# Optimization experiments

Hardware: AMD Instinct MI355X
Metric: run time of the kernel (lower is better)

## Reference

```python
import jax, jax.numpy as jnp
import numpy as np

N, Z_DIM = 131072, 64
K_CODES = 2048
QUANT_TEMP = 0.0  # default T when 'quant_temp' not passed


def setup_inputs() -> dict:
    key = jax.random.key(0)
    k1, k2 = jax.random.split(key)
    z = jax.random.normal(k1, (N, Z_DIM), dtype=jnp.float32)
    e = jax.random.normal(k2, (K_CODES, Z_DIM), dtype=jnp.float32)
    return {"z": z, "e": e}


def reference(z, e):
    # torch.cdist -> euclidean distance matrix [N, K]; argmin over squared
    # distance gives identical indices (sqrt is monotone), so skip the sqrt.
    # ||z - e||^2 = ||z||^2 - 2 z.e^T + ||e||^2
    z_sq = jnp.sum(z * z, axis=1, keepdims=True)          # [N, 1]
    e_sq = jnp.sum(e * e, axis=1)                          # [K]
    d2 = z_sq - 2.0 * (z @ e.T) + e_sq[None, :]            # [N, K]
    min_indices = jnp.argmin(d2, axis=1)                   # [N] int
    z_q = e[min_indices]                                   # gather [N, Z]
    commit_loss = jnp.mean((z - z_q) ** 2)                 # F.mse_loss
    # straight-through: z + (1 - T) * stop_grad(z_q - z), T = 0
    z_out = z + (1.0 - QUANT_TEMP) * jax.lax.stop_gradient(z_q - z)
    return z_out, min_indices, commit_loss
```

## Files before the change

kernel.cpp:

```cpp
#include <hip/hip_runtime.h>


#define N_ROWS 131072
#define ZD 64
#define KCODES 2048
#define RF 4
#define EPS_S 0.02f
#define FLAG_CAP 65536
#define RFIX 8

using f16x8   = __attribute__((ext_vector_type(8))) _Float16;
using floatx4 = __attribute__((ext_vector_type(4))) float;


__global__ void prep_kernel(const float* __restrict__ e, float* __restrict__ ws) {
    int t = threadIdx.x, lane = t & 63, w = t >> 6;
    if (blockIdx.x == 0 && t == 0) { ws[0] = 0.0f; ((unsigned int*)ws)[1] = 0u; }
    int c = blockIdx.x * 4 + w;
    float* esn = ws + 1024;
    double* esq64 = (double*)((char*)ws + 16384);
    unsigned short* et = (unsigned short*)((char*)ws + 32768);
    float* eT = (float*)((char*)ws + 557056);

    float x = e[(size_t)c * ZD + lane];
    union { _Float16 h; unsigned short u; } cv;
    cv.h = (_Float16)x;
    int base = ((c >> 4) << 10) + ((lane >> 3) << 7) + ((c & 15) << 3) + (lane & 7);
    et[base] = cv.u;
    eT[lane * KCODES + c] = x;
    double s = (double)x * (double)x;
    for (int off = 1; off < 64; off <<= 1) s += __shfl_xor(s, off, 64);
    if (lane == 0) { esq64[c] = s; esn[c] = (float)(-0.5 * s); }
}

#define COMPUTE(H0, H1, EN, FCOL) do {                                       \
    floatx4 _ai = {EN, EN, EN, EN};                                          \
    _Pragma("unroll")                                                        \
    for (int _rf = 0; _rf < RF; _rf++) {                                     \
        floatx4 acc;                                                         \
        acc = __builtin_amdgcn_mfma_f32_16x16x32_f16(Fh[_rf][0], H0, _ai, 0, 0, 0); \
        acc = __builtin_amdgcn_mfma_f32_16x16x32_f16(Fh[_rf][1], H1, acc, 0, 0, 0); \
        _Pragma("unroll")                                                    \
        for (int _r = 0; _r < 4; _r++) {                                     \
            float _s  = acc[_r];                                             \
            bool  _gt = _s > mval[_rf][_r];                                  \
            mv2[_rf][_r]  = __builtin_amdgcn_fmed3f(_s, mval[_rf][_r], mv2[_rf][_r]); \
            midx[_rf][_r] = _gt ? (FCOL) : midx[_rf][_r];                    \
            mval[_rf][_r] = fmaxf(_s, mval[_rf][_r]);                        \
        }                                                                    \
    }                                                                        \
} while (0)

#define STAGEP(BUF, P) do {                                                  \
    const char* _src = etiles + ((size_t)((P) & 63) << 12)                   \
                       + ((size_t)threadIdx.x << 4);                         \
    __builtin_amdgcn_global_load_lds(                                        \
        (const __attribute__((address_space(1))) unsigned int*)_src,         \
        (__attribute__((address_space(3))) unsigned int*)&tilebuf[BUF][w << 10], \
        16, 0, 0);                                                           \
} while (0)

#define ITER_R(CT) do {                                                      \
    STAGEP(((CT) + 2) & 3, (CT) + 2);                                        \
    asm volatile("s_waitcnt vmcnt(2)" ::: "memory");                         \
    __builtin_amdgcn_s_barrier();                                            \
    float _en0 = esn_sm[(CT) * 32 + lrow];                                   \
    float _en1 = esn_sm[(CT) * 32 + 16 + lrow];                              \
    const char* _tb = tilebuf[(CT) & 3];                                     \
    f16x8 h0, h1;                                                            \
    h0 = *(const f16x8*)(const void*)(_tb + (lane << 4));                    \
    h1 = *(const f16x8*)(const void*)(_tb + 1024 + (lane << 4));             \
    COMPUTE(h0, h1, _en0, fcol);                                             \
    fcol += 16.0f;                                                           \
    h0 = *(const f16x8*)(const void*)(_tb + 2048 + (lane << 4));             \
    h1 = *(const f16x8*)(const void*)(_tb + 3072 + (lane << 4));             \
    COMPUTE(h0, h1, _en1, fcol);                                             \
    fcol += 16.0f;                                                           \
} while (0)

__global__ __launch_bounds__(256, 2) void vq_mfma(
        const float* __restrict__ z, const float* __restrict__ e,
        float* __restrict__ ws, float* __restrict__ out) {
    const char* etiles = (const char*)ws + 32768;
    unsigned int* cntp  = (unsigned int*)ws + 1;
    unsigned int* flags = (unsigned int*)((char*)ws + 294912);

    __shared__ __attribute__((aligned(16))) char tilebuf[4][4096];
    __shared__ __attribute__((aligned(16))) float esn_sm[KCODES];

    int lane = threadIdx.x & 63;
    int w    = threadIdx.x >> 6;
    int wid  = blockIdx.x * 4 + w;
    int row0 = wid * (RF * 16);
    int lrow = lane & 15;
    int lq   = lane >> 4;

    f16x8 Fh[RF][2];
#pragma unroll
    for (int rf = 0; rf < RF; rf++)
#pragma unroll
        for (int kc = 0; kc < 2; kc++) {
            const float* zp = z + (size_t)(row0 + rf * 16 + lrow) * ZD + kc * 32 + lq * 8;
            float xv[8];
            *(float4*)(void*)&xv[0] = *(const float4*)(const void*)zp;
            *(float4*)(void*)&xv[4] = *(const float4*)(const void*)(zp + 4);
            f16x8 h;
#pragma unroll
            for (int j = 0; j < 8; j++) h[j] = (_Float16)xv[j];
            Fh[rf][kc] = h;
            asm volatile("" : "+v"(Fh[rf][kc]));
        }
    asm volatile("s_waitcnt vmcnt(0)" ::: "memory");

    {
        const char* esrc = (const char*)ws + 4096 + ((size_t)threadIdx.x << 4);
        __builtin_amdgcn_global_load_lds(
            (const __attribute__((address_space(1))) unsigned int*)esrc,
            (__attribute__((address_space(3))) unsigned int*)((char*)esn_sm + (w << 10)),
            16, 0, 0);
        __builtin_amdgcn_global_load_lds(
            (const __attribute__((address_space(1))) unsigned int*)(esrc + 4096),
            (__attribute__((address_space(3))) unsigned int*)((char*)esn_sm + 4096 + (w << 10)),
            16, 0, 0);
    }
    STAGEP(0, 0);
    STAGEP(1, 1);

    floatx4 mval[RF], mv2[RF], midx[RF];
#pragma unroll
    for (int rf = 0; rf < RF; rf++)
#pragma unroll
        for (int r = 0; r < 4; r++) {
            mval[rf][r] = -3.0e38f; mv2[rf][r] = -3.0e38f; midx[rf][r] = 0.0f;
        }

    float fcol = (float)lrow;

    for (int ct = 0; ct < 64; ct += 4) {
        ITER_R(ct);
        ITER_R(ct + 1);
        ITER_R(ct + 2);
        ITER_R(ct + 3);
    }

    float lacc = 0.0f;
#pragma unroll
    for (int rf = 0; rf < RF; rf++)
#pragma unroll
        for (int r = 0; r < 4; r++) {
            float v = mval[rf][r], v2 = mv2[rf][r], fi = midx[rf][r];
            for (int off = 1; off < 16; off <<= 1) {
                float ov  = __shfl_xor(v,  off, 64);
                float ofi = __shfl_xor(fi, off, 64);
                float ov2 = __shfl_xor(v2, off, 64);
                bool take = (ov > v) || ((ov == v) && (ofi < fi));
                float loser = take ? v : ov;
                v2 = fmaxf(fmaxf(v2, ov2), loser);
                v  = take ? ov  : v;
                fi = take ? ofi : fi;
            }
            int row = row0 + rf * 16 + lq * 4 + r;
            int idx = (int)fi;
            float4 ev = ((const float4*)(const void*)(e + (size_t)idx * ZD))[lrow];
            float4 zv = ((const float4*)(const void*)(z + (size_t)row * ZD))[lrow];
            ((float4*)(void*)(out + (size_t)row * ZD))[lrow] = ev;
            float dx = ev.x - zv.x, dy = ev.y - zv.y;
            float dz = ev.z - zv.z, dw = ev.w - zv.w;
            lacc = fmaf(dx, dx, lacc); lacc = fmaf(dy, dy, lacc);
            lacc = fmaf(dz, dz, lacc); lacc = fmaf(dw, dw, lacc);
            if (lrow == 0) {
                out[(size_t)N_ROWS * ZD + row] = fi;
                if (v - v2 < EPS_S) {
                    unsigned int i = atomicAdd(cntp, 1u);
                    if (i < FLAG_CAP) flags[i] = (unsigned int)row;
                }
            }
        }

    for (int off = 1; off < 64; off <<= 1) lacc += __shfl_xor(lacc, off, 64);
    __shared__ float sm[4];
    if (lane == 0) sm[w] = lacc;
    __syncthreads();
    if (threadIdx.x == 0) atomicAdd(ws, sm[0] + sm[1] + sm[2] + sm[3]);
}

__global__ __launch_bounds__(256) void vq_fixup(
        const float* __restrict__ z, const float* __restrict__ e,
        float* __restrict__ ws, float* __restrict__ out) {
    const double* esq64 = (const double*)((const char*)ws + 16384);
    const float* eT = (const float*)((const char*)ws + 557056);
    const unsigned int* flags = (const unsigned int*)((const char*)ws + 294912);
    unsigned int cnt = ((const unsigned int*)ws)[1];
    bool allrows = cnt > FLAG_CAP;
    unsigned int n = allrows ? N_ROWS : cnt;

    if (blockIdx.x == 0 && threadIdx.x == 0)
        out[(size_t)N_ROWS * ZD + N_ROWS] = ws[0] * (1.0f / 8388608.0f);
    if (n == 0) return;

    __shared__ float zrow[RFIX][ZD];
    __shared__ int rows_sm[RFIX];
    __shared__ double sd[4][RFIX]; __shared__ int si[4][RFIX];
    __shared__ int sbest[RFIX];
    int t = threadIdx.x, lane = t & 63, w = t >> 6;

    unsigned int ngroups = (n + RFIX - 1) / RFIX;
    for (unsigned int g = blockIdx.x; g < ngroups; g += gridDim.x) {
        __syncthreads();
        if (t < RFIX) {
            unsigned int u = g * RFIX + (unsigned int)t;
            if (u >= n) u = n - 1;
            rows_sm[t] = allrows ? (int)u : (int)flags[u];
        }
        __syncthreads();
        zrow[t >> 6][t & 63]       = z[(size_t)rows_sm[t >> 6] * ZD + (t & 63)];
        zrow[4 + (t >> 6)][t & 63] = z[(size_t)rows_sm[4 + (t >> 6)] * ZD + (t & 63)];
        __syncthreads();

        double dacc[8][RFIX];
#pragma unroll
        for (int j = 0; j < 8; j++)
#pragma unroll
            for (int r = 0; r < RFIX; r++) dacc[j][r] = 0.0;

        for (int k = 0; k < ZD; k++) {
            const float* ek = eT + k * KCODES + t;
            float e8[8];
#pragma unroll
            for (int j = 0; j < 8; j++) e8[j] = ek[256 * j];
#pragma unroll
            for (int r = 0; r < RFIX; r++) {
                double zk = (double)zrow[r][k];
#pragma unroll
                for (int j = 0; j < 8; j++)
                    dacc[j][r] = fma(zk, (double)e8[j], dacc[j][r]);
            }
        }

#pragma unroll
        for (int r = 0; r < RFIX; r++) {
            double dmin = 1.0e300; int imin = 0;
#pragma unroll
            for (int j = 0; j < 8; j++) {
                int c = t + 256 * j;
                double d = fma(-2.0, dacc[j][r], esq64[c]);
                if (d < dmin) { dmin = d; imin = c; }
            }
            for (int off = 1; off < 64; off <<= 1) {
                double od = __shfl_xor(dmin, off, 64);
                int    oi = __shfl_xor(imin, off, 64);
                if (od < dmin || (od == dmin && oi < imin)) { dmin = od; imin = oi; }
            }
            if (lane == 0) { sd[w][r] = dmin; si[w][r] = imin; }
        }
        __syncthreads();
        if (t < RFIX) {
            double bd = sd[0][t]; int bi = si[0][t];
            for (int q = 1; q < 4; q++)
                if (sd[q][t] < bd || (sd[q][t] == bd && si[q][t] < bi)) {
                    bd = sd[q][t]; bi = si[q][t];
                }
            sbest[t] = bi;
        }
        __syncthreads();
        if (t < 16 * RFIX) {
            int r = t >> 4, pos = t & 15;
            unsigned int u = g * RFIX + (unsigned int)r;
            if (u < n) {
                int row = rows_sm[r]; int bi = sbest[r];
                ((float4*)(void*)(out + (size_t)row * ZD))[pos] =
                    ((const float4*)(const void*)(e + (size_t)bi * ZD))[pos];
                if (pos == 0) out[(size_t)N_ROWS * ZD + row] = (float)bi;
            }
        }
    }
}

extern "C" void kernel_launch(void* const* d_in, const int* in_sizes, int n_in,
                              void* d_out, int out_size, void* d_ws, size_t ws_size,
                              hipStream_t stream) {
    const float* z = (const float*)d_in[0];
    const float* e = (const float*)d_in[1];
    float* out = (float*)d_out;
    float* ws  = (float*)d_ws;

    prep_kernel<<<dim3(512), dim3(256), 0, stream>>>(e, ws);
    vq_mfma<<<dim3(512), dim3(256), 0, stream>>>(z, e, ws, out);
    vq_fixup<<<dim3(1024), dim3(256), 0, stream>>>(z, e, ws, out);
}
```

Before: 192.0 us.

## Tile codebook prep through shared memory and halve fixup rows per group

The codebook prep kernel now stages a 64-code tile in padded shared memory. From that tile it writes the transposed fp32 copy with coalesced stores and the fp16 MFMA layout with 16-byte packed stores, and it computes the squared norms serially per thread instead of with wave shuffles. It launches 32 blocks instead of 512. The fixup kernel now handles 4 flagged rows per group instead of 8, which lowers register pressure from the double accumulators but reads the codebook more often per flagged row.

```diff
diff --git a/kernel.cpp b/kernel.cpp
--- a/kernel.cpp
+++ b/kernel.cpp
@@ -7,30 +7,61 @@
 #define RF 4
 #define EPS_S 0.02f
 #define FLAG_CAP 65536
-#define RFIX 8
+#define RFIX 4
 
 using f16x8   = __attribute__((ext_vector_type(8))) _Float16;
 using floatx4 = __attribute__((ext_vector_type(4))) float;
 
 
-__global__ void prep_kernel(const float* __restrict__ e, float* __restrict__ ws) {
-    int t = threadIdx.x, lane = t & 63, w = t >> 6;
+__global__ __launch_bounds__(256) void prep_kernel(
+        const float* __restrict__ e, float* __restrict__ ws) {
+    __shared__ float tile[64][65];
+    int t = threadIdx.x;
+    int c0 = blockIdx.x * 64;
     if (blockIdx.x == 0 && t == 0) { ws[0] = 0.0f; ((unsigned int*)ws)[1] = 0u; }
-    int c = blockIdx.x * 4 + w;
+
     float* esn = ws + 1024;
     double* esq64 = (double*)((char*)ws + 16384);
     unsigned short* et = (unsigned short*)((char*)ws + 32768);
     float* eT = (float*)((char*)ws + 557056);
 
-    float x = e[(size_t)c * ZD + lane];
-    union { _Float16 h; unsigned short u; } cv;
-    cv.h = (_Float16)x;
-    int base = ((c >> 4) << 10) + ((lane >> 3) << 7) + ((c & 15) << 3) + (lane & 7);
-    et[base] = cv.u;
-    eT[lane * KCODES + c] = x;
-    double s = (double)x * (double)x;
-    for (int off = 1; off < 64; off <<= 1) s += __shfl_xor(s, off, 64);
-    if (lane == 0) { esq64[c] = s; esn[c] = (float)(-0.5 * s); }
+#pragma unroll
+    for (int i = 0; i < 16; i++) {
+        int idx = i * 256 + t;
+        int cc = idx >> 6, k = idx & 63;
+        tile[cc][k] = e[(size_t)(c0 + cc) * ZD + k];
+    }
+    __syncthreads();
+
+    if (t < 64) {
+        double s = 0.0;
+#pragma unroll
+        for (int k = 0; k < 64; k++) { double v = (double)tile[t][k]; s = fma(v, v, s); }
+        esq64[c0 + t] = s;
+        esn[c0 + t] = (float)(-0.5 * s);
+    }
+
+#pragma unroll
+    for (int i = 0; i < 16; i++) {
+        int idx = i * 256 + t;
+        int k = idx >> 6, cc = idx & 63;
+        eT[(size_t)k * KCODES + c0 + cc] = tile[cc][k];
+    }
+
+#pragma unroll
+    for (int i = 0; i < 2; i++) {
+        int h = i * 256 + t;
+        int tl   = h >> 7;
+        int kb   = (h >> 4) & 7;
+        int code = h & 15;
+        int row  = tl * 16 + code;
+        union { _Float16 hf[8]; unsigned int u32[4]; } pk;
+#pragma unroll
+        for (int j = 0; j < 8; j++) pk.hf[j] = (_Float16)tile[row][kb * 8 + j];
+        int gtile = (c0 >> 4) + tl;
+        unsigned int* dst = (unsigned int*)(et + (size_t)gtile * 1024 + kb * 128 + code * 8);
+        *(uint4*)(void*)dst = *(uint4*)(void*)pk.u32;
+    }
 }
 
 #define COMPUTE(H0, H1, EN, FCOL) do {                                       \
@@ -213,8 +244,7 @@
             rows_sm[t] = allrows ? (int)u : (int)flags[u];
         }
         __syncthreads();
-        zrow[t >> 6][t & 63]       = z[(size_t)rows_sm[t >> 6] * ZD + (t & 63)];
-        zrow[4 + (t >> 6)][t & 63] = z[(size_t)rows_sm[4 + (t >> 6)] * ZD + (t & 63)];
+        zrow[t >> 6][t & 63] = z[(size_t)rows_sm[t >> 6] * ZD + (t & 63)];
         __syncthreads();
 
         double dacc[8][RFIX];
@@ -284,7 +314,7 @@
     float* out = (float*)d_out;
     float* ws  = (float*)d_ws;
 
-    prep_kernel<<<dim3(512), dim3(256), 0, stream>>>(e, ws);
+    prep_kernel<<<dim3(32), dim3(256), 0, stream>>>(e, ws);
     vq_mfma<<<dim3(512), dim3(256), 0, stream>>>(z, e, ws, out);
     vq_fixup<<<dim3(1024), dim3(256), 0, stream>>>(z, e, ws, out);
 }
```

Measured after the change: 180.5 us. 6.0% less time.
